# Optimization experiments

Measured on AMD Instinct MI355X. Metric: run time of the kernel, lower is better.

Reference implementation:

```python
import jax, jax.numpy as jnp
import numpy as np

B, N, DIM_IN, DIM_K, DIM_V, NH = 2, 2048, 1024, 1024, 1024, 16

def setup_inputs() -> dict:
    key = jax.random.key(0)
    ks = jax.random.split(key, 7)
    s_in = 1.0 / np.sqrt(DIM_IN)
    return {
        "x": jax.random.normal(ks[0], (B, N, DIM_IN), dtype=jnp.float32),
        "Wq": jax.random.uniform(ks[1], (DIM_IN, DIM_K), jnp.float32, -s_in, s_in),
        "bq": jax.random.uniform(ks[2], (DIM_K,), jnp.float32, -s_in, s_in),
        "Wk": jax.random.uniform(ks[3], (DIM_IN, DIM_K), jnp.float32, -s_in, s_in),
        "bk": jax.random.uniform(ks[4], (DIM_K,), jnp.float32, -s_in, s_in),
        "Wv": jax.random.uniform(ks[5], (DIM_IN, DIM_V), jnp.float32, -s_in, s_in),
        "bv": jax.random.uniform(ks[6], (DIM_V,), jnp.float32, -s_in, s_in),
    }

def reference(x, Wq, bq, Wk, bk, Wv, bv):
    b, n, _ = x.shape
    dk = DIM_K // NH
    dv = DIM_V // NH
    scale = 1.0 / np.sqrt(dk)
    # project and split heads: [b, nh, n, dk]
    q = (x @ Wq + bq).reshape(b, n, NH, dk).transpose(0, 2, 1, 3)
    k = (x @ Wk + bk).reshape(b, n, NH, dk).transpose(0, 2, 1, 3)
    v = (x @ Wv + bv).reshape(b, n, NH, dv).transpose(0, 2, 1, 3)
    dist = jnp.einsum('bhqd,bhkd->bhqk', q, k) * scale  # [b,nh,n,n]
    dist = jax.nn.softmax(dist, axis=-1)
    att = jnp.einsum('bhqk,bhkd->bhqd', dist, v)
    return att.transpose(0, 2, 1, 3).reshape(b, n, DIM_V)
```

## Files before the change

### kernel.cpp

```cpp
#include <hip/hip_runtime.h>

#define DI __device__ __forceinline__

typedef unsigned short u16;
typedef short short8 __attribute__((ext_vector_type(8)));
typedef float f32x2 __attribute__((ext_vector_type(2)));
typedef float f32x4 __attribute__((ext_vector_type(4)));
typedef float f32x16 __attribute__((ext_vector_type(16)));
typedef u16 u16x4 __attribute__((ext_vector_type(4)));
typedef unsigned u32x4 __attribute__((ext_vector_type(4)));
typedef int i32x2 __attribute__((ext_vector_type(2)));

DI u16 f2bf(float f){
    unsigned u = __builtin_bit_cast(unsigned, f);
    u += 0x7FFFu + ((u >> 16) & 1u);
    return (u16)(u >> 16);
}

#if defined(__has_builtin)
#if __has_builtin(__builtin_amdgcn_global_load_lds)
#define HAS_GLL 1
#endif
#if __has_builtin(__builtin_amdgcn_exp2f)
#define HAS_EXP2 1
#endif
#if __has_builtin(__builtin_amdgcn_permlane32_swap)
#define HAS_PL32 1
#endif
#endif

DI void async16(u16* lds, const u16* g){
#ifdef HAS_GLL
    __builtin_amdgcn_global_load_lds(
        (const __attribute__((address_space(1))) unsigned int*)g,
        (__attribute__((address_space(3))) unsigned int*)lds, 16, 0, 0);
#else
    *(short8*)lds = *(const short8*)g;
#endif
}

DI float ex2(float x){
#ifdef HAS_EXP2
    return __builtin_amdgcn_exp2f(x);
#else
    return exp2f(x);
#endif
}

DI unsigned cvtpk(float lo, float hi){
    unsigned r;
    asm("v_cvt_pk_bf16_f32 %0, %1, %2" : "=v"(r) : "v"(lo), "v"(hi));
    return r;
}

DI i32x2 plswap(int a, int b){
#ifdef HAS_PL32
    return __builtin_amdgcn_permlane32_swap(a, b, false, false);
#else
    i32x2 r;
    int ax = __shfl_xor(a, 32), bx = __shfl_xor(b, 32);
    int hi = (threadIdx.x & 63) >> 5;
    r[0] = hi ? bx : a;
    r[1] = hi ? b : ax;
    return r;
#endif
}

#define SEQ   2048
#define DIN   1024
#define MTOT  4096
#define QSCALE 0.18033688011112042f

__global__ void k_cvt_x(const float* __restrict__ x, u16* __restrict__ xb){
    int i = (blockIdx.x * 256 + threadIdx.x) * 4;
    f32x4 v = *(const f32x4*)(x + i);
    u16x4 o;
    for (int j = 0; j < 4; j++) o[j] = f2bf(v[j]);
    *(u16x4*)(xb + i) = o;
}

__global__ void k_tw3(const float* __restrict__ Wq, const float* __restrict__ Wk,
                      const float* __restrict__ Wv, u16* __restrict__ Wt3){
    const float* W = (blockIdx.z == 0) ? Wq : (blockIdx.z == 1) ? Wk : Wv;
    u16* Wt = Wt3 + (size_t)blockIdx.z * DIN * DIN;
    __shared__ float t[32][33];
    int tx = threadIdx.x, ty = threadIdx.y;
    int n0 = blockIdx.x * 32, k0 = blockIdx.y * 32;
    for (int i = 0; i < 4; i++)
        t[ty + i*8][tx] = W[(size_t)(k0 + ty + i*8) * DIN + n0 + tx];
    __syncthreads();
    for (int i = 0; i < 4; i++)
        Wt[(size_t)(n0 + ty + i*8) * DIN + k0 + tx] = f2bf(t[tx][ty + i*8]);
}

__global__ __launch_bounds__(256, 3) void k_projf(const u16* __restrict__ A,
                                                  const u16* __restrict__ Wt3,
                                                  const float* __restrict__ bq,
                                                  const float* __restrict__ bk,
                                                  const float* __restrict__ bv,
                                                  u16* __restrict__ qb,
                                                  u16* __restrict__ kb,
                                                  u16* __restrict__ vtb){
    __shared__ __align__(16) u16 As[3][4096];
    __shared__ __align__(16) u16 Bs[3][4096];
    int tid = threadIdx.x;
    int l = tid & 63, w = tid >> 6;
    int lq = l & 15, lg = l >> 4;
    int wm = w >> 1, wn = w & 1;
    int by  = blockIdx.y;
    int mat = by >> 3;
    int m0 = blockIdx.x * 128, n0 = (by & 7) * 128;
    const u16* Bt = Wt3 + (size_t)mat * DIN * DIN;
    const float* bias = (mat == 0) ? bq : (mat == 1) ? bk : bv;

    int r0 = tid >> 2, c0 = (tid & 3) * 8;
    const u16* ap0 = A  + (size_t)(m0 + r0)      * DIN + c0;
    const u16* ap1 = A  + (size_t)(m0 + 64 + r0) * DIN + c0;
    const u16* bp0 = Bt + (size_t)(n0 + r0)      * DIN + c0;
    const u16* bp1 = Bt + (size_t)(n0 + 64 + r0) * DIN + c0;
    int d0 = tid * 8, d1 = 2048 + tid * 8;

#define PSTAGE(bi) {                                              \
    async16(&As[bi][d0], ap0); async16(&As[bi][d1], ap1);         \
    async16(&Bs[bi][d0], bp0); async16(&Bs[bi][d1], bp1);         \
    ap0 += 32; ap1 += 32; bp0 += 32; bp1 += 32; }

    f32x4 acc[4][4] = {};
    PSTAGE(0)
    PSTAGE(1)

    for (int t = 0; t < 32; t++){
        int cur = t % 3;
        if (t + 2 < 32) PSTAGE((t + 2) % 3)
        if (t < 30)      asm volatile("s_waitcnt vmcnt(8)" ::: "memory");
        else if (t == 30) asm volatile("s_waitcnt vmcnt(4)" ::: "memory");
        else              asm volatile("s_waitcnt vmcnt(0)" ::: "memory");
        __builtin_amdgcn_s_barrier();

        short8 af[4], bf[4];
        #pragma unroll
        for (int f = 0; f < 4; f++){
            af[f] = *(const short8*)&As[cur][(wm*64 + f*16 + lq) * 32 + lg * 8];
            bf[f] = *(const short8*)&Bs[cur][(wn*64 + f*16 + lq) * 32 + lg * 8];
        }
        __builtin_amdgcn_s_setprio(1);
        #pragma unroll
        for (int fm = 0; fm < 4; fm++)
            #pragma unroll
            for (int fn = 0; fn < 4; fn++)
                acc[fm][fn] = __builtin_amdgcn_mfma_f32_16x16x32_bf16(af[fm], bf[fn], acc[fm][fn], 0, 0, 0);
        __builtin_amdgcn_s_setprio(0);
        __builtin_amdgcn_s_barrier();
    }
#undef PSTAGE

    if (mat == 2){
        for (int fn = 0; fn < 4; fn++){
            int cc = n0 + wn*64 + fn*16 + lq;
            float bvv = bias[cc];
            int hh = cc >> 6, d = cc & 63;
            for (int fm = 0; fm < 4; fm++){
                int mbase = m0 + wm*64 + fm*16 + lg*4;
                int b = mbase >> 11, n = mbase & 2047;
                u16x4 pv;
                for (int r = 0; r < 4; r++) pv[r] = f2bf(acc[fm][fn][r] + bvv);
                *(u16x4*)&vtb[((size_t)(b*16 + hh) * 64 + d) * SEQ + n] = pv;
            }
        }
    } else {
        u16* dst = (mat == 0) ? qb : kb;
        float sc = (mat == 0) ? QSCALE : 1.0f;
        u16* Cs = &As[0][0];
        float bvv[4];
        #pragma unroll
        for (int fn = 0; fn < 4; fn++) bvv[fn] = bias[n0 + wn*64 + fn*16 + lq];

        for (int fm = 0; fm < 4; fm++){
            __syncthreads();
            #pragma unroll
            for (int fn = 0; fn < 4; fn++){
                int c = wn*64 + fn*16 + lq;
                #pragma unroll
                for (int r = 0; r < 4; r++)
                    Cs[(wm*16 + lg*4 + r)*136 + c] = f2bf((acc[fm][fn][r] + bvv[fn]) * sc);
            }
            __syncthreads();
            #pragma unroll
            for (int j = 0; j < 2; j++){
                int wr = (tid >> 4) + j*16;
                int coloff = (tid & 15) * 8;
                int ng = m0 + (wr >> 4)*64 + fm*16 + (wr & 15);
                int b = ng >> 11, n = ng & 2047;
                int cg = n0 + coloff;
                int hh = cg >> 6, d = cg & 63;
                *(short8*)&dst[((size_t)(b*16 + hh) * SEQ + n) * 64 + d] =
                    *(const short8*)&Cs[wr*136 + coloff];
            }
        }
    }
}

#define MFMA32(a, b, c) __builtin_amdgcn_mfma_f32_32x32x16_bf16(a, b, c, 0, 0, 0)

#define MAKE_PA(dst, S, base) {                                   \
    unsigned a0 = cvtpk(S[base+0], S[base+1]);                    \
    unsigned a1 = cvtpk(S[base+2], S[base+3]);                    \
    unsigned b0 = cvtpk(S[base+4], S[base+5]);                    \
    unsigned b1 = cvtpk(S[base+6], S[base+7]);                    \
    i32x2 r0 = plswap((int)a0, (int)b0);                          \
    i32x2 r1 = plswap((int)a1, (int)b1);                          \
    u32x4 wv = {(unsigned)r0[0], (unsigned)r1[0],                 \
                (unsigned)r0[1], (unsigned)r1[1]};                \
    dst = __builtin_bit_cast(short8, wv); }

template<int SPLIT>
__global__ __launch_bounds__(256, 4) void k_attn(const u16* __restrict__ Q,
                                                 const u16* __restrict__ K,
                                                 const u16* __restrict__ Vt,
                                                 float* __restrict__ out,
                                                 float* __restrict__ po,
                                                 float* __restrict__ mls){
    __shared__ __align__(16) u16 Ks[2][64 * 64];
    __shared__ __align__(16) u16 Vs[2][64 * 64];

    int tid = threadIdx.x, l = tid & 63, w = tid >> 6;
    int lq = l & 31, hi = l >> 5;
    int bh = blockIdx.y;
    int b = bh >> 4, h = bh & 15;
    int q0 = blockIdx.x * 128 + w * 32;
    int sp = blockIdx.z;
    int kvb = sp * (SEQ / SPLIT);
    const int NT = (SEQ / SPLIT) / 64;

    const u16* Qb = Q  + (size_t)bh * SEQ * 64;
    const u16* Kb = K  + (size_t)bh * SEQ * 64;
    const u16* Vb = Vt + (size_t)bh * 64 * SEQ;

    int row0 = tid >> 3;
    int c0   = (tid & 7) ^ (row0 & 7);
    const u16* kp0 = Kb + (size_t)(kvb + row0)      * 64 + c0 * 8;
    const u16* kp1 = Kb + (size_t)(kvb + row0 + 32) * 64 + c0 * 8;
    const u16* vp0 = Vb + (size_t)row0        * SEQ + kvb + c0 * 8;
    const u16* vp1 = Vb + (size_t)(row0 + 32) * SEQ + kvb + c0 * 8;
    int d0 = tid * 8, d1 = 2048 + tid * 8;

#define STAGE(bi) {                                               \
    async16(&Ks[bi][d0], kp0); async16(&Ks[bi][d1], kp1);         \
    async16(&Vs[bi][d0], vp0); async16(&Vs[bi][d1], vp1);         \
    kp0 += 64*64; kp1 += 64*64; vp0 += 64; vp1 += 64; }

    short8 qf[4];
    #pragma unroll
    for (int ks = 0; ks < 4; ks++)
        qf[ks] = *(const short8*)(Qb + (size_t)(q0 + lq) * 64 + ks*16 + hi*8);

    STAGE(0)

    float m = 0.f;
    float ls = 0.f;
    f32x16 o0 = {}, o1 = {};
    int rx = (lq & 7) << 4;

    for (int t = 0; t < NT; t++){
        int cur = t & 1;
        if (t + 1 < NT) STAGE(cur ^ 1)
        if (t == 0){
            if (NT > 1) asm volatile("s_waitcnt vmcnt(4)" ::: "memory");
            else        asm volatile("s_waitcnt vmcnt(0)" ::: "memory");
            __builtin_amdgcn_s_barrier();
        }

        const char* kB = (const char*)&Ks[cur][0];
        const char* vB = (const char*)&Vs[cur][0];

        f32x16 st0 = {}, st1 = {};
        __builtin_amdgcn_s_setprio(1);
        #pragma unroll
        for (int ks = 0; ks < 4; ks++){
            int cb = ((ks*2 + hi) << 4) ^ rx;
            short8 ka = *(const short8*)(kB + lq*128        + cb);
            short8 kb = *(const short8*)(kB + (32+lq)*128   + cb);
            st0 = MFMA32(ka, qf[ks], st0);
            st1 = MFMA32(kb, qf[ks], st1);
        }
        __builtin_amdgcn_s_setprio(0);

        if (m != 0.f){
            #pragma unroll
            for (int r = 0; r < 16; r++){ st0[r] -= m; st1[r] -= m; }
        }

        f32x2 ps = {0.f, 0.f};
        #pragma unroll
        for (int r = 0; r < 16; r += 2){
            st0[r]   = ex2(st0[r]);
            st0[r+1] = ex2(st0[r+1]);
            st1[r]   = ex2(st1[r]);
            st1[r+1] = ex2(st1[r+1]);
            f32x2 a = {st0[r], st0[r+1]};
            f32x2 c = {st1[r], st1[r+1]};
            ps += a + c;
        }
        float psum = ps[0] + ps[1];
        psum += __shfl_xor(psum, 32);

        short8 pa0, pa1, pa2, pa3;
        MAKE_PA(pa0, st0, 0)
        MAKE_PA(pa1, st0, 8)
        MAKE_PA(pa2, st1, 0)
        MAKE_PA(pa3, st1, 8)

        __builtin_amdgcn_s_setprio(1);
        #pragma unroll
        for (int kct = 0; kct < 4; kct++){
            short8 pf = (kct == 0) ? pa0 : (kct == 1) ? pa1 : (kct == 2) ? pa2 : pa3;
            int cb = ((kct*2 + hi) << 4) ^ rx;
            short8 v0 = *(const short8*)(vB + lq*128      + cb);
            short8 v1 = *(const short8*)(vB + (32+lq)*128 + cb);
            o0 = MFMA32(pf, v0, o0);
            o1 = MFMA32(pf, v1, o1);
        }
        __builtin_amdgcn_s_setprio(0);

        ls += psum;
        if (__any(ls > 1.0e30f)){
            const float dn = 5.421010862427522e-20f;
            ls *= dn;
            #pragma unroll
            for (int r = 0; r < 16; r++){ o0[r] *= dn; o1[r] *= dn; }
            m += 64.f;
        }

        asm volatile("s_waitcnt vmcnt(0)" ::: "memory");
        __builtin_amdgcn_s_barrier();
    }

    if (SPLIT == 1){
        #pragma unroll
        for (int r = 0; r < 16; r++){
            int row = (r & 3) + 8*(r >> 2) + 4*hi;
            float inv = 1.0f / __shfl(ls, row);
            float* op = out + ((size_t)b * SEQ + (q0 + row)) * 1024 + h*64 + lq;
            op[0]  = o0[r] * inv;
            op[32] = o1[r] * inv;
        }
    } else {
        float* pb = po + (size_t)sp * MTOT * 1024;
        #pragma unroll
        for (int r = 0; r < 16; r++){
            int row = (r & 3) + 8*(r >> 2) + 4*hi;
            float* op = pb + ((size_t)b * SEQ + (q0 + row)) * 1024 + h*64 + lq;
            op[0]  = o0[r];
            op[32] = o1[r];
        }
        if (hi == 0){
            float* mp = mls + (((size_t)sp*32 + bh) * SEQ + (q0 + lq)) * 2;
            mp[0] = m; mp[1] = ls;
        }
    }
#undef STAGE
}

template<int S>
__global__ __launch_bounds__(256) void k_comb(const float* __restrict__ po,
                                              const float* __restrict__ mls,
                                              float* __restrict__ out){
    size_t i = ((size_t)blockIdx.x * 256 + threadIdx.x) * 4;
    size_t row = i >> 10;
    int col = (int)(i & 1023);
    int b = (int)(row >> 11), n = (int)(row & 2047);
    int bh = b*16 + (col >> 6);

    float mv[S], lv[S], wv[S];
    float M = -INFINITY;
    #pragma unroll
    for (int s = 0; s < S; s++){
        const float* p = mls + (((size_t)s*32 + bh) * SEQ + n) * 2;
        mv[s] = p[0]; lv[s] = p[1];
        M = fmaxf(M, mv[s]);
    }
    float L = 0.f;
    #pragma unroll
    for (int s = 0; s < S; s++){ wv[s] = ex2(mv[s] - M); L += wv[s] * lv[s]; }
    float inv = 1.0f / L;
    f32x4 acc = {};
    #pragma unroll
    for (int s = 0; s < S; s++){
        f32x4 v = *(const f32x4*)(po + (size_t)s * MTOT * 1024 + i);
        acc += v * wv[s];
    }
    acc *= inv;
    *(f32x4*)(out + i) = acc;
}

extern "C" void kernel_launch(void* const* d_in, const int* in_sizes, int n_in,
                              void* d_out, int out_size, void* d_ws, size_t ws_size,
                              hipStream_t stream){
    const float* x  = (const float*)d_in[0];
    const float* Wq = (const float*)d_in[1];
    const float* bq = (const float*)d_in[2];
    const float* Wk = (const float*)d_in[3];
    const float* bk = (const float*)d_in[4];
    const float* Wv = (const float*)d_in[5];
    const float* bv = (const float*)d_in[6];
    float* out = (float*)d_out;

    const size_t MB = (size_t)1 << 20;
    if (ws_size < 38 * MB) return;

    char* ws = (char*)d_ws;
    u16* xb   = (u16*)(ws);
    u16* wt3  = (u16*)(ws +  8 * MB);
    u16* qb   = (u16*)(ws + 14 * MB);
    u16* kb   = (u16*)(ws + 22 * MB);
    u16* vtb  = (u16*)(ws + 30 * MB);
    int S = (ws_size >= 38 * MB + 2 * 17 * MB) ? 2 : 1;
    float* po  = (float*)(ws + 38 * MB);
    float* mls = (float*)(ws + 38 * MB + (size_t)S * 16 * MB);

    k_cvt_x<<<4096, 256, 0, stream>>>(x, xb);
    k_tw3<<<dim3(32, 32, 3), dim3(32, 8), 0, stream>>>(Wq, Wk, Wv, wt3);

    k_projf<<<dim3(32, 24), 256, 0, stream>>>(xb, wt3, bq, bk, bv, qb, kb, vtb);

    if (S == 2){
        k_attn<2><<<dim3(16, 32, 2), 256, 0, stream>>>(qb, kb, vtb, out, po, mls);
        k_comb<2><<<4096, 256, 0, stream>>>(po, mls, out);
    } else {
        k_attn<1><<<dim3(16, 32, 1), 256, 0, stream>>>(qb, kb, vtb, out, po, mls);
    }
}
```

Before: 102.6 us.

## Merge input prep kernels and store split-attention partials in bf16

Folds the x-to-bf16 conversion and the weight transpose into a single launch, removing one kernel launch. The split-KV attention partial outputs are now written as bf16 instead of fp32, which halves the bytes written by attention and read by the combine kernel. The workspace requirement for the two-way split drops, so the split path is more likely to be selected. In exchange the unnormalized partial outputs are rounded to bf16 before combining, which adds some precision loss.

```diff
diff --git a/kernel.cpp b/kernel.cpp
--- a/kernel.cpp
+++ b/kernel.cpp
@@ -15,6 +15,10 @@
     unsigned u = __builtin_bit_cast(unsigned, f);
     u += 0x7FFFu + ((u >> 16) & 1u);
     return (u16)(u >> 16);
+}
+DI float bf2f(u16 b){
+    unsigned u = ((unsigned)b) << 16;
+    return __builtin_bit_cast(float, u);
 }
 
 #if defined(__has_builtin)
@@ -71,26 +75,35 @@
 #define MTOT  4096
 #define QSCALE 0.18033688011112042f
 
-__global__ void k_cvt_x(const float* __restrict__ x, u16* __restrict__ xb){
-    int i = (blockIdx.x * 256 + threadIdx.x) * 4;
-    f32x4 v = *(const f32x4*)(x + i);
-    u16x4 o;
-    for (int j = 0; j < 4; j++) o[j] = f2bf(v[j]);
-    *(u16x4*)(xb + i) = o;
-}
-
-__global__ void k_tw3(const float* __restrict__ Wq, const float* __restrict__ Wk,
-                      const float* __restrict__ Wv, u16* __restrict__ Wt3){
-    const float* W = (blockIdx.z == 0) ? Wq : (blockIdx.z == 1) ? Wk : Wv;
-    u16* Wt = Wt3 + (size_t)blockIdx.z * DIN * DIN;
+__global__ void k_prep(const float* __restrict__ x,
+                       const float* __restrict__ Wq, const float* __restrict__ Wk,
+                       const float* __restrict__ Wv,
+                       u16* __restrict__ xb, u16* __restrict__ Wt3){
     __shared__ float t[32][33];
-    int tx = threadIdx.x, ty = threadIdx.y;
-    int n0 = blockIdx.x * 32, k0 = blockIdx.y * 32;
-    for (int i = 0; i < 4; i++)
-        t[ty + i*8][tx] = W[(size_t)(k0 + ty + i*8) * DIN + n0 + tx];
-    __syncthreads();
-    for (int i = 0; i < 4; i++)
-        Wt[(size_t)(n0 + ty + i*8) * DIN + k0 + tx] = f2bf(t[tx][ty + i*8]);
+    int bid = blockIdx.x, tid = threadIdx.x;
+    if (bid < 4096){
+        int i = (bid * 256 + tid) * 4;
+        f32x4 v = *(const f32x4*)(x + i);
+        u16x4 o;
+        #pragma unroll
+        for (int j = 0; j < 4; j++) o[j] = f2bf(v[j]);
+        *(u16x4*)(xb + i) = o;
+    } else {
+        int tb = bid - 4096;
+        int z  = tb >> 10;
+        int t2 = tb & 1023;
+        const float* W = (z == 0) ? Wq : (z == 1) ? Wk : Wv;
+        u16* Wt = Wt3 + (size_t)z * DIN * DIN;
+        int tx = tid & 31, ty = tid >> 5;
+        int n0 = (t2 & 31) * 32, k0 = (t2 >> 5) * 32;
+        #pragma unroll
+        for (int i = 0; i < 4; i++)
+            t[ty + i*8][tx] = W[(size_t)(k0 + ty + i*8) * DIN + n0 + tx];
+        __syncthreads();
+        #pragma unroll
+        for (int i = 0; i < 4; i++)
+            Wt[(size_t)(n0 + ty + i*8) * DIN + k0 + tx] = f2bf(t[tx][ty + i*8]);
+    }
 }
 
 __global__ __launch_bounds__(256, 3) void k_projf(const u16* __restrict__ A,
@@ -218,7 +231,7 @@
                                                  const u16* __restrict__ K,
                                                  const u16* __restrict__ Vt,
                                                  float* __restrict__ out,
-                                                 float* __restrict__ po,
+                                                 u16* __restrict__ po,
                                                  float* __restrict__ mls){
     __shared__ __align__(16) u16 Ks[2][64 * 64];
     __shared__ __align__(16) u16 Vs[2][64 * 64];
@@ -345,13 +358,13 @@
             op[32] = o1[r] * inv;
         }
     } else {
-        float* pb = po + (size_t)sp * MTOT * 1024;
+        u16* pb = po + (size_t)sp * MTOT * 1024;
         #pragma unroll
         for (int r = 0; r < 16; r++){
             int row = (r & 3) + 8*(r >> 2) + 4*hi;
-            float* op = pb + ((size_t)b * SEQ + (q0 + row)) * 1024 + h*64 + lq;
-            op[0]  = o0[r];
-            op[32] = o1[r];
+            u16* op = pb + ((size_t)b * SEQ + (q0 + row)) * 1024 + h*64 + lq;
+            op[0]  = f2bf(o0[r]);
+            op[32] = f2bf(o1[r]);
         }
         if (hi == 0){
             float* mp = mls + (((size_t)sp*32 + bh) * SEQ + (q0 + lq)) * 2;
@@ -362,7 +375,7 @@
 }
 
 template<int S>
-__global__ __launch_bounds__(256) void k_comb(const float* __restrict__ po,
+__global__ __launch_bounds__(256) void k_comb(const u16* __restrict__ po,
                                               const float* __restrict__ mls,
                                               float* __restrict__ out){
     size_t i = ((size_t)blockIdx.x * 256 + threadIdx.x) * 4;
@@ -386,8 +399,9 @@
     f32x4 acc = {};
     #pragma unroll
     for (int s = 0; s < S; s++){
-        f32x4 v = *(const f32x4*)(po + (size_t)s * MTOT * 1024 + i);
-        acc += v * wv[s];
+        u16x4 v = *(const u16x4*)(po + (size_t)s * MTOT * 1024 + i);
+        #pragma unroll
+        for (int j = 0; j < 4; j++) acc[j] += wv[s] * bf2f(v[j]);
     }
     acc *= inv;
     *(f32x4*)(out + i) = acc;
@@ -414,12 +428,11 @@
     u16* qb   = (u16*)(ws + 14 * MB);
     u16* kb   = (u16*)(ws + 22 * MB);
     u16* vtb  = (u16*)(ws + 30 * MB);
-    int S = (ws_size >= 38 * MB + 2 * 17 * MB) ? 2 : 1;
-    float* po  = (float*)(ws + 38 * MB);
-    float* mls = (float*)(ws + 38 * MB + (size_t)S * 16 * MB);
-
-    k_cvt_x<<<4096, 256, 0, stream>>>(x, xb);
-    k_tw3<<<dim3(32, 32, 3), dim3(32, 8), 0, stream>>>(Wq, Wk, Wv, wt3);
+    int S = (ws_size >= 38 * MB + 2 * 9 * MB) ? 2 : 1;
+    u16* po    = (u16*)(ws + 38 * MB);
+    float* mls = (float*)(ws + 38 * MB + (size_t)S * 8 * MB);
+
+    k_prep<<<7168, 256, 0, stream>>>(x, Wq, Wk, Wv, xb, wt3);
 
     k_projf<<<dim3(32, 24), 256, 0, stream>>>(xb, wt3, bq, bk, bv, qb, kb, vtb);
 
```

Measured after the change: 97.52 us. 5.0% less time.
